# Kernel tuning notes

Measured on AMD Instinct MI355X. Metric: run time of the kernel, lower is better.

Reference implementation:

```python
import jax, jax.numpy as jnp
import numpy as np

M, B, S = 8, 64, 1024
I = K = V = 256
H = 8
F = 1024


def setup_inputs() -> dict:
    key0 = jax.random.key(0)
    ks = iter(jax.random.split(key0, 64))
    nrm = lambda shp, s=1.0: jax.random.normal(next(ks), shp, dtype=jnp.float32) * s
    w = 0.05
    inp = {
        's0': nrm((M, B, I)), 'q0': nrm((M, B, K)), 'k0': nrm((M, B, K)), 'v0': nrm((M, B, V)),
        'key': nrm((S, B, K)), 'value': nrm((S, B, V)),
        'attn_wq': nrm((M, K, K), w), 'attn_wk': nrm((M, K, K), w), 'attn_wv': nrm((M, K, K), w),
        'attn_bq': nrm((M, K), w), 'attn_bk': nrm((M, K), w), 'attn_bv': nrm((M, K), w),
        'attn_wo': nrm((M, K, K), w), 'attn_bo': nrm((M, K), w),
    }
    for p, out in (('q', K), ('k', K), ('v', V), ('s', I)):
        inp[p + '_w1'] = nrm((M, 2 * I, F), w)
        inp[p + '_b1'] = nrm((M, F), w)
        inp[p + '_w2'] = nrm((M, F, out), w)
        inp[p + '_b2'] = nrm((M, out), w)
    inp['g_w1'] = nrm((4, M, 2 * I, F), w)
    inp['g_b1'] = nrm((4, M, F), w)
    inp['g_w2'] = nrm((4, M, F, 1), w)
    inp['g_b2'] = nrm((4, M, 1), w)
    return inp


def _forward(s0, q0, k0, v0, key, value,
             attn_wq, attn_wk, attn_wv, attn_bq, attn_bk, attn_bv, attn_wo, attn_bo,
             q_w1, q_b1, q_w2, q_b2, k_w1, k_b1, k_w2, k_b2,
             v_w1, v_b1, v_w2, v_b2, s_w1, s_b1, s_w2, s_b2,
             g_w1, g_b1, g_w2, g_b2):
    m, b, kd = q0.shape
    s = key.shape[0]
    hd = kd // H
    # per-module projections (single-query decode-style attention)
    q = jnp.einsum('mbk,mkd->mbd', q0, attn_wq) + attn_bq[:, None, :]          # (M,B,K)
    kk = jnp.einsum('sbk,mkd->msbd', key, attn_wk) + attn_bk[:, None, None, :]  # (M,S,B,K)
    vv = jnp.einsum('sbk,mkd->msbd', value, attn_wv) + attn_bv[:, None, None, :]
    qh = q.reshape(m, b, H, hd)
    kh = kk.reshape(m, s, b, H, hd)
    vh = vv.reshape(m, s, b, H, hd)
    scores = jnp.einsum('mbhd,msbhd->mbhs', qh, kh) / jnp.sqrt(jnp.float32(hd))
    aw = jax.nn.softmax(scores, axis=-1)                                        # (M,B,H,S)
    ctx = jnp.einsum('mbhs,msbhd->mbhd', aw, vh).reshape(m, b, kd)
    attn_out = jnp.einsum('mbk,mko->mbo', ctx, attn_wo) + attn_bo[:, None, :]   # (M,B,K)
    attn_weights = aw.mean(axis=2)                                              # (M,B,S)

    # _make_mlp puts ReLU FIRST: Seq(ReLU, Lin, ReLU, Lin, last_act)
    fc_in = jax.nn.relu(jnp.concatenate([attn_out, s0], axis=-1))               # (M,B,2I)

    def head(w1, b1, w2, b2):
        h = jax.nn.relu(jnp.einsum('mbi,mif->mbf', fc_in, w1) + b1[:, None, :])
        return jnp.einsum('mbf,mfo->mbo', h, w2) + b2[:, None, :]

    # non-gate heads: last activation ReLU, then .tanh() in forward
    oq = jnp.tanh(jax.nn.relu(head(q_w1, q_b1, q_w2, q_b2)))
    ok = jnp.tanh(jax.nn.relu(head(k_w1, k_b1, k_w2, k_b2)))
    ov = jnp.tanh(jax.nn.relu(head(v_w1, v_b1, v_w2, v_b2)))
    os_ = jnp.tanh(jax.nn.relu(head(s_w1, s_b1, s_w2, s_b2)))

    # gate heads stacked on leading g axis (query,key,value,state)
    gh = jax.nn.relu(jnp.einsum('mbi,gmif->gmbf', fc_in, g_w1) + g_b1[:, :, None, :])
    gates = jax.nn.sigmoid(jnp.einsum('gmbf,gmfo->gmbo', gh, g_w2) + g_b2[:, :, None, :])
    qg, kg, vg, sg = gates[0], gates[1], gates[2], gates[3]

    gq = qg * oq + (1.0 - qg) * q0
    gk = kg * ok + (1.0 - kg) * k0
    gv = vg * ov + (1.0 - vg) * v0
    gs = sg * os_ + (1.0 - sg) * s0
    return attn_out, attn_weights, gs, gq, gk, gv


def reference(s0, q0, k0, v0, key, value,
              attn_wq, attn_wk, attn_wv, attn_bq, attn_bk, attn_bv, attn_wo, attn_bo,
              q_w1, q_b1, q_w2, q_b2, k_w1, k_b1, k_w2, k_b2,
              v_w1, v_b1, v_w2, v_b2, s_w1, s_b1, s_w2, s_b2,
              g_w1, g_b1, g_w2, g_b2):
    return _forward(s0, q0, k0, v0, key, value,
                    attn_wq, attn_wk, attn_wv, attn_bq, attn_bk, attn_bv, attn_wo, attn_bo,
                    q_w1, q_b1, q_w2, q_b2, k_w1, k_b1, k_w2, k_b2,
                    v_w1, v_b1, v_w2, v_b2, s_w1, s_b1, s_w2, s_b2,
                    g_w1, g_b1, g_w2, g_b2)
```

## Files before the change

kernel.cpp:

```cpp
#include <hip/hip_runtime.h>
#include <math.h>

#define Mm 8
#define Bb 64
#define Ss 1024
#define Kk 256
#define Hh 8
#define HD 32
#define Ff 1024

typedef _Float16 f16x8 __attribute__((ext_vector_type(8)));
typedef float f32x4 __attribute__((ext_vector_type(4)));

#define WS_Q      0u
#define WS_U      131072u
#define WS_QDB    1179648u
#define WS_SC     1183744u
#define WS_WPART  5378048u
#define WS_FC     0u
#define WS_H1     5378048u
#define WS_GATES  262144u
#define WS_HPART  1183744u

__device__ __forceinline__ void dma16(const float* g, float* l) {
  __builtin_amdgcn_global_load_lds(
      (const __attribute__((address_space(1))) unsigned int*)g,
      (__attribute__((address_space(3))) unsigned int*)l, 16, 0, 0);
}

__device__ __forceinline__ f16x8 frag_ctg(const float* T, int r, int quad) {
  const int x = r & 7;
  const float4 a0 = *(const float4*)&T[r * 32 + (((2 * quad) ^ x) << 2)];
  const float4 a1 = *(const float4*)&T[r * 32 + (((2 * quad + 1) ^ x) << 2)];
  f16x8 f;
  f[0] = (_Float16)a0.x; f[1] = (_Float16)a0.y;
  f[2] = (_Float16)a0.z; f[3] = (_Float16)a0.w;
  f[4] = (_Float16)a1.x; f[5] = (_Float16)a1.y;
  f[6] = (_Float16)a1.z; f[7] = (_Float16)a1.w;
  return f;
}

__device__ __forceinline__ int swz(int kr) {
  return (kr & 15) ^ ((kr >> 3) << 1);
}
__device__ __forceinline__ f16x8 frag_ctr(const float* T, int col, int quad) {
  const int g = col >> 2, c = col & 3;
  f16x8 f;
#pragma unroll
  for (int j = 0; j < 8; ++j) {
    const int kr = quad * 8 + j;
    f[j] = (_Float16)T[kr * 64 + ((g ^ swz(kr)) << 2) + c];
  }
  return f;
}

__global__ __launch_bounds__(256) void k1_qproj(
    const float* __restrict__ q0, const float* __restrict__ wq,
    const float* __restrict__ bq, float* __restrict__ qout) {
  __shared__ float q0s[8 * 260];
  const int m = blockIdx.x, b0 = blockIdx.y * 8, t = threadIdx.x;
#pragma unroll
  for (int j = 0; j < 8; ++j)
    q0s[j * 260 + t] = q0[(m * Bb + b0 + j) * Kk + t];
  __syncthreads();
  float acc[8];
  const float bias = bq[m * Kk + t];
#pragma unroll
  for (int j = 0; j < 8; ++j) acc[j] = bias;
  const float* wcol = wq + m * Kk * Kk + t;
  for (int k4 = 0; k4 < Kk / 4; ++k4) {
    const float w0 = wcol[(k4 * 4 + 0) * Kk];
    const float w1 = wcol[(k4 * 4 + 1) * Kk];
    const float w2 = wcol[(k4 * 4 + 2) * Kk];
    const float w3 = wcol[(k4 * 4 + 3) * Kk];
#pragma unroll
    for (int j = 0; j < 8; ++j) {
      const float4 qv = *(const float4*)&q0s[j * 260 + k4 * 4];
      acc[j] += qv.x * w0 + qv.y * w1 + qv.z * w2 + qv.w * w3;
    }
  }
#pragma unroll
  for (int j = 0; j < 8; ++j)
    qout[(m * Bb + b0 + j) * Kk + t] = acc[j];
}

__global__ __launch_bounds__(256) void k2_uproj(
    const float* __restrict__ wk, const float* __restrict__ bk,
    const float* __restrict__ q, float* __restrict__ u,
    float* __restrict__ qdb) {
  __shared__ float qs[64 * 36];
  const int m = blockIdx.x, h = blockIdx.y, t = threadIdx.x;
#pragma unroll
  for (int p = 0; p < 8; ++p) {
    const int idx = p * 256 + t;
    const int d = idx & 31, b = idx >> 5;
    qs[b * 36 + d] = q[(m * Bb + b) * Kk + h * HD + d];
  }
  __syncthreads();
  float acc[64];
#pragma unroll
  for (int b = 0; b < 64; ++b) acc[b] = 0.f;
  const float* wrow = wk + (m * Kk + t) * Kk + h * HD;
#pragma unroll
  for (int d4 = 0; d4 < 8; ++d4) {
    const float4 w4 = *(const float4*)&wrow[d4 * 4];
#pragma unroll
    for (int b = 0; b < 64; ++b) {
      const float4 q4 = *(const float4*)&qs[b * 36 + d4 * 4];
      acc[b] += q4.x * w4.x + q4.y * w4.y + q4.z * w4.z + q4.w * w4.w;
    }
  }
  for (int b = 0; b < 64; ++b)
    u[((m * Bb + b) * Hh + h) * Kk + t] = acc[b];
  if (t < 64) {
    float s = 0.f;
#pragma unroll
    for (int d = 0; d < 32; ++d)
      s += qs[t * 36 + d] * bk[m * Kk + h * HD + d];
    qdb[(m * Bb + t) * Hh + h] = s;
  }
}

__global__ __launch_bounds__(256) void k3_scores(
    const float* __restrict__ key, const float* __restrict__ u,
    const float* __restrict__ qdb, float* __restrict__ sc) {
  __shared__ __attribute__((aligned(16))) float TA[2][2048];
  __shared__ __attribute__((aligned(16))) float TB[2][2048];
  __shared__ float qd[64];
  const int b = blockIdx.x, st0 = blockIdx.y * 64, t = threadIdx.x;
  const int w = t >> 6, lane = t & 63, quad = (t >> 4) & 3, l15 = t & 15;
  if (t < 64) qd[t] = qdb[((t >> 3) * Bb + b) * Hh + (t & 7)];

  auto dmaAB = [&](int c, int buf) {
#pragma unroll
    for (int j = 0; j < 2; ++j) {
      const int r = w * 16 + j * 8 + (lane >> 3);
      const int gp = (lane & 7) ^ (r & 7);
      dma16(u + (((r >> 3) * Bb + b) * Hh + (r & 7)) * Kk + c * 32 + gp * 4,
            &TA[buf][(w * 2 + j) * 256 + lane * 4]);
    }
#pragma unroll
    for (int j = 0; j < 2; ++j) {
      const int sr = w * 16 + j * 8 + (lane >> 3);
      const int gp = (lane & 7) ^ (sr & 7);
      dma16(key + (size_t)(st0 + sr) * (Bb * Kk) + b * Kk + c * 32 + gp * 4,
            &TB[buf][(w * 2 + j) * 256 + lane * 4]);
    }
  };

  f32x4 acc[4];
#pragma unroll
  for (int i = 0; i < 4; ++i) acc[i] = (f32x4){0.f, 0.f, 0.f, 0.f};
  dmaAB(0, 0);
  __syncthreads();
#pragma unroll
  for (int c = 0; c < 8; ++c) {
    if (c + 1 < 8) dmaAB(c + 1, (c + 1) & 1);
    const float* A = TA[c & 1];
    const float* B = TB[c & 1];
    const f16x8 af = frag_ctg(A, w * 16 + l15, quad);
#pragma unroll
    for (int sf = 0; sf < 4; ++sf) {
      const f16x8 bf = frag_ctg(B, sf * 16 + l15, quad);
      acc[sf] =
          __builtin_amdgcn_mfma_f32_16x16x32_f16(af, bf, acc[sf], 0, 0, 0);
    }
    __syncthreads();
  }
  const float scale = 0.17677669529663687f;
#pragma unroll
  for (int sf = 0; sf < 4; ++sf) {
    const int s = st0 + sf * 16 + l15;
#pragma unroll
    for (int r = 0; r < 4; ++r) {
      const int mh = w * 16 + quad * 4 + r;
      sc[(size_t)(((mh >> 3) * Bb + b) * Hh + (mh & 7)) * Ss + s] =
          (acc[sf][r] + qd[mh]) * scale;
    }
  }
}

__global__ __launch_bounds__(256) void k3b_softmax(float* __restrict__ sc,
                                                   float* __restrict__ out) {
  __shared__ float rows[8 * 1024];
  const int m = blockIdx.x, b = blockIdx.y, t = threadIdx.x;
  const int w = t >> 6, lane = t & 63;
  const size_t base = (size_t)(m * Bb + b) * (Hh * Ss);
#pragma unroll
  for (int hh = 0; hh < 2; ++hh) {
    const int h = w * 2 + hh;
    float* g = sc + base + h * 1024;
    float4 v0 = *(const float4*)&g[lane * 4];
    float4 v1 = *(const float4*)&g[256 + lane * 4];
    float4 v2 = *(const float4*)&g[512 + lane * 4];
    float4 v3 = *(const float4*)&g[768 + lane * 4];
    float mx = fmaxf(fmaxf(fmaxf(v0.x, v0.y), fmaxf(v0.z, v0.w)),
                     fmaxf(fmaxf(v1.x, v1.y), fmaxf(v1.z, v1.w)));
    mx = fmaxf(mx, fmaxf(fmaxf(fmaxf(v2.x, v2.y), fmaxf(v2.z, v2.w)),
                         fmaxf(fmaxf(v3.x, v3.y), fmaxf(v3.z, v3.w))));
#pragma unroll
    for (int off = 32; off > 0; off >>= 1)
      mx = fmaxf(mx, __shfl_xor(mx, off, 64));
    v0.x = __expf(v0.x - mx); v0.y = __expf(v0.y - mx);
    v0.z = __expf(v0.z - mx); v0.w = __expf(v0.w - mx);
    v1.x = __expf(v1.x - mx); v1.y = __expf(v1.y - mx);
    v1.z = __expf(v1.z - mx); v1.w = __expf(v1.w - mx);
    v2.x = __expf(v2.x - mx); v2.y = __expf(v2.y - mx);
    v2.z = __expf(v2.z - mx); v2.w = __expf(v2.w - mx);
    v3.x = __expf(v3.x - mx); v3.y = __expf(v3.y - mx);
    v3.z = __expf(v3.z - mx); v3.w = __expf(v3.w - mx);
    float sm = v0.x + v0.y + v0.z + v0.w + v1.x + v1.y + v1.z + v1.w +
               v2.x + v2.y + v2.z + v2.w + v3.x + v3.y + v3.z + v3.w;
#pragma unroll
    for (int off = 32; off > 0; off >>= 1) sm += __shfl_xor(sm, off, 64);
    const float inv = 1.f / sm;
    v0.x *= inv; v0.y *= inv; v0.z *= inv; v0.w *= inv;
    v1.x *= inv; v1.y *= inv; v1.z *= inv; v1.w *= inv;
    v2.x *= inv; v2.y *= inv; v2.z *= inv; v2.w *= inv;
    v3.x *= inv; v3.y *= inv; v3.z *= inv; v3.w *= inv;
    *(float4*)&g[lane * 4] = v0;
    *(float4*)&g[256 + lane * 4] = v1;
    *(float4*)&g[512 + lane * 4] = v2;
    *(float4*)&g[768 + lane * 4] = v3;
    float* r = rows + h * 1024;
    *(float4*)&r[lane * 4] = v0;
    *(float4*)&r[256 + lane * 4] = v1;
    *(float4*)&r[512 + lane * 4] = v2;
    *(float4*)&r[768 + lane * 4] = v3;
  }
  __syncthreads();
#pragma unroll
  for (int p = 0; p < 4; ++p) {
    const int s = p * 256 + t;
    float sum = 0.f;
#pragma unroll
    for (int h = 0; h < 8; ++h) sum += rows[h * 1024 + s];
    out[131072u + (m * Bb + b) * Ss + s] = sum * 0.125f;
  }
}

__global__ __launch_bounds__(256) void k4a_av(const float* __restrict__ value,
                                              const float* __restrict__ aw,
                                              float* __restrict__ wpart) {
  __shared__ __attribute__((aligned(16))) float TA[2][2048];
  __shared__ __attribute__((aligned(16))) float TB[2][2048];
  const int b = blockIdx.x, ko = blockIdx.y, sq = blockIdx.z, t = threadIdx.x;
  const int w = t >> 6, lane = t & 63, quad = (t >> 4) & 3, l15 = t & 15;

  auto dmaAB = [&](int c, int buf) {
#pragma unroll
    for (int j = 0; j < 2; ++j) {
      const int r = w * 16 + j * 8 + (lane >> 3);
      const int gp = (lane & 7) ^ (r & 7);
      dma16(aw + ((size_t)((r >> 3) * Bb + b) * Hh + (r & 7)) * Ss +
                sq * 256 + c * 32 + gp * 4,
            &TA[buf][(w * 2 + j) * 256 + lane * 4]);
    }
#pragma unroll
    for (int j = 0; j < 2; ++j) {
      const int kr = w * 8 + j * 4 + (lane >> 4);
      const int gp = (lane & 15) ^ swz(kr);
      dma16(value + (size_t)(sq * 256 + c * 32 + kr) * (Bb * Kk) + b * Kk +
                ko * 64 + gp * 4,
            &TB[buf][(w * 2 + j) * 256 + lane * 4]);
    }
  };

  f32x4 acc[4];
#pragma unroll
  for (int i = 0; i < 4; ++i) acc[i] = (f32x4){0.f, 0.f, 0.f, 0.f};
  dmaAB(0, 0);
  __syncthreads();
#pragma unroll
  for (int c = 0; c < 8; ++c) {
    if (c + 1 < 8) dmaAB(c + 1, (c + 1) & 1);
    const float* A = TA[c & 1];
    const float* B = TB[c & 1];
    const f16x8 af = frag_ctg(A, w * 16 + l15, quad);
#pragma unroll
    for (int nf = 0; nf < 4; ++nf) {
      const f16x8 bf = frag_ctr(B, nf * 16 + l15, quad);
      acc[nf] =
          __builtin_amdgcn_mfma_f32_16x16x32_f16(af, bf, acc[nf], 0, 0, 0);
    }
    __syncthreads();
  }
  float* wp = wpart + sq * 1048576u;
#pragma unroll
  for (int nf = 0; nf < 4; ++nf) {
    const int k = ko * 64 + nf * 16 + l15;
#pragma unroll
    for (int r = 0; r < 4; ++r) {
      const int mh = w * 16 + quad * 4 + r;
      wp[((size_t)((mh >> 3) * Bb + b) * Hh + (mh & 7)) * Kk + k] =
          acc[nf][r];
    }
  }
}

__global__ __launch_bounds__(256) void k5_ctx(
    const float* __restrict__ wv, const float* __restrict__ bv,
    const float* __restrict__ wo, const float* __restrict__ bo,
    const float* __restrict__ s0in, const float* __restrict__ wpart,
    float* __restrict__ attn_out, float* __restrict__ fc) {
  __shared__ float wsh[2048];
  __shared__ float ctxs[256];
  const int m = blockIdx.x, b = blockIdx.y, t = threadIdx.x;
  const int base = (m * Bb + b) * (Hh * Kk);
#pragma unroll
  for (int p = 0; p < 8; ++p) {
    const int o = base + p * 256 + t;
    wsh[p * 256 + t] = wpart[o] + wpart[1048576u + o] + wpart[2097152u + o] +
                       wpart[3145728u + o];
  }
  __syncthreads();
  const int h = t >> 5;
  float acc = bv[m * Kk + t];
  const float* wvc = wv + m * Kk * Kk + t;
  for (int k4 = 0; k4 < 64; ++k4) {
    const float4 a4 = *(const float4*)&wsh[h * 256 + k4 * 4];
    acc += a4.x * wvc[(k4 * 4 + 0) * Kk] + a4.y * wvc[(k4 * 4 + 1) * Kk] +
           a4.z * wvc[(k4 * 4 + 2) * Kk] + a4.w * wvc[(k4 * 4 + 3) * Kk];
  }
  ctxs[t] = acc;
  __syncthreads();
  float acc2 = bo[m * Kk + t];
  const float* woc = wo + m * Kk * Kk + t;
  for (int k4 = 0; k4 < 64; ++k4) {
    const float4 c4 = *(const float4*)&ctxs[k4 * 4];
    acc2 += c4.x * woc[(k4 * 4 + 0) * Kk] + c4.y * woc[(k4 * 4 + 1) * Kk] +
            c4.z * woc[(k4 * 4 + 2) * Kk] + c4.w * woc[(k4 * 4 + 3) * Kk];
  }
  const int ob = (m * Bb + b) * Kk + t;
  attn_out[ob] = acc2;
  fc[(m * Bb + b) * 512 + t] = fmaxf(acc2, 0.f);
  fc[(m * Bb + b) * 512 + 256 + t] = fmaxf(s0in[ob], 0.f);
}

__global__ __launch_bounds__(256) void k6_mlp1(
    const float* __restrict__ fc, const float* __restrict__ w1q,
    const float* __restrict__ w1k, const float* __restrict__ w1v,
    const float* __restrict__ w1s, const float* __restrict__ w1g,
    const float* __restrict__ b1q, const float* __restrict__ b1k,
    const float* __restrict__ b1v, const float* __restrict__ b1s,
    const float* __restrict__ b1g, float* __restrict__ h1) {
  __shared__ __attribute__((aligned(16))) float TA[2][2048];
  __shared__ __attribute__((aligned(16))) float TB[2][2048];
  const int ft = blockIdx.x, m = blockIdx.y, head = blockIdx.z,
            t = threadIdx.x;
  const float* w1;
  const float* b1;
  if (head == 0)      { w1 = w1q; b1 = b1q; }
  else if (head == 1) { w1 = w1k; b1 = b1k; }
  else if (head == 2) { w1 = w1v; b1 = b1v; }
  else if (head == 3) { w1 = w1s; b1 = b1s; }
  else {
    w1 = w1g + (size_t)(head - 4) * (Mm * 512 * Ff);
    b1 = b1g + (head - 4) * (Mm * Ff);
  }
  w1 += (size_t)m * 512 * Ff;
  b1 += m * Ff;
  const int w = t >> 6, lane = t & 63, quad = (t >> 4) & 3, l15 = t & 15;
  const float* fcm = fc + m * Bb * 512;

  auto dmaAB = [&](int c, int buf) {
#pragma unroll
    for (int j = 0; j < 2; ++j) {
      const int r = w * 16 + j * 8 + (lane >> 3);
      const int gp = (lane & 7) ^ (r & 7);
      dma16(fcm + r * 512 + c * 32 + gp * 4,
            &TA[buf][(w * 2 + j) * 256 + lane * 4]);
    }
#pragma unroll
    for (int j = 0; j < 2; ++j) {
      const int kr = w * 8 + j * 4 + (lane >> 4);
      const int gp = (lane & 15) ^ swz(kr);
      dma16(w1 + (size_t)(c * 32 + kr) * Ff + ft * 64 + gp * 4,
            &TB[buf][(w * 2 + j) * 256 + lane * 4]);
    }
  };

  f32x4 acc[4];
#pragma unroll
  for (int i = 0; i < 4; ++i) acc[i] = (f32x4){0.f, 0.f, 0.f, 0.f};
  dmaAB(0, 0);
  __syncthreads();
#pragma unroll
  for (int c = 0; c < 16; ++c) {
    if (c + 1 < 16) dmaAB(c + 1, (c + 1) & 1);
    const float* A = TA[c & 1];
    const float* B = TB[c & 1];
    const f16x8 bf = frag_ctr(B, w * 16 + l15, quad);
#pragma unroll
    for (int mt = 0; mt < 4; ++mt) {
      const f16x8 af = frag_ctg(A, mt * 16 + l15, quad);
      acc[mt] =
          __builtin_amdgcn_mfma_f32_16x16x32_f16(af, bf, acc[mt], 0, 0, 0);
    }
    __syncthreads();
  }
  const int f = ft * 64 + w * 16 + l15;
  const float bias = b1[f];
  float* hb = h1 + (size_t)((head * Mm + m) * Bb) * Ff + f;
#pragma unroll
  for (int mt = 0; mt < 4; ++mt) {
#pragma unroll
    for (int r = 0; r < 4; ++r) {
      const int bb = mt * 16 + quad * 4 + r;
      hb[(size_t)bb * Ff] = fmaxf(acc[mt][r] + bias, 0.f);
    }
  }
}

__global__ __launch_bounds__(64) void k6b_gates(
    const float* __restrict__ h1, const float* __restrict__ gw2,
    const float* __restrict__ gb2, float* __restrict__ gates) {
  const int gm = blockIdx.x, b = blockIdx.y, t = threadIdx.x;
  const int g = gm >> 3, m = gm & 7;
  const float* hrow = h1 + (size_t)(((4 + g) * Mm + m) * Bb + b) * Ff;
  const float* wrow = gw2 + (g * Mm + m) * Ff;
  float s = 0.f;
#pragma unroll
  for (int i = 0; i < 16; ++i) s += hrow[t + i * 64] * wrow[t + i * 64];
  for (int off = 32; off > 0; off >>= 1) s += __shfl_down(s, off, 64);
  if (t == 0)
    gates[(g * Mm + m) * Bb + b] =
        1.f / (1.f + __expf(-(s + gb2[g * Mm + m])));
}

__global__ __launch_bounds__(256) void k7a_mlp2(
    const float* __restrict__ h1, const float* __restrict__ w2q,
    const float* __restrict__ w2k, const float* __restrict__ w2v,
    const float* __restrict__ w2s, float* __restrict__ hpart) {
  __shared__ __attribute__((aligned(16))) float TA[2][2048];
  __shared__ __attribute__((aligned(16))) float TB[2][2048];
  const int ot = blockIdx.x & 3, fq = blockIdx.x >> 2;
  const int m = blockIdx.y, head = blockIdx.z, t = threadIdx.x;
  const float* w2 =
      (head == 0) ? w2q : (head == 1) ? w2k : (head == 2) ? w2v : w2s;
  w2 += (size_t)m * Ff * Kk;
  const int w = t >> 6, lane = t & 63, quad = (t >> 4) & 3, l15 = t & 15;
  const float* hbase = h1 + (size_t)((head * Mm + m) * Bb) * Ff + fq * 256;

  auto dmaAB = [&](int c, int buf) {
#pragma unroll
    for (int j = 0; j < 2; ++j) {
      const int r = w * 16 + j * 8 + (lane >> 3);
      const int gp = (lane & 7) ^ (r & 7);
      dma16(hbase + (size_t)r * Ff + c * 32 + gp * 4,
            &TA[buf][(w * 2 + j) * 256 + lane * 4]);
    }
#pragma unroll
    for (int j = 0; j < 2; ++j) {
      const int kr = w * 8 + j * 4 + (lane >> 4);
      const int gp = (lane & 15) ^ swz(kr);
      dma16(w2 + (size_t)(fq * 256 + c * 32 + kr) * Kk + ot * 64 + gp * 4,
            &TB[buf][(w * 2 + j) * 256 + lane * 4]);
    }
  };

  f32x4 acc[4];
#pragma unroll
  for (int i = 0; i < 4; ++i) acc[i] = (f32x4){0.f, 0.f, 0.f, 0.f};
  dmaAB(0, 0);
  __syncthreads();
#pragma unroll
  for (int c = 0; c < 8; ++c) {
    if (c + 1 < 8) dmaAB(c + 1, (c + 1) & 1);
    const float* A = TA[c & 1];
    const float* B = TB[c & 1];
    const f16x8 bf = frag_ctr(B, w * 16 + l15, quad);
#pragma unroll
    for (int mt = 0; mt < 4; ++mt) {
      const f16x8 af = frag_ctg(A, mt * 16 + l15, quad);
      acc[mt] =
          __builtin_amdgcn_mfma_f32_16x16x32_f16(af, bf, acc[mt], 0, 0, 0);
    }
    __syncthreads();
  }
  const int o = ot * 64 + w * 16 + l15;
  float* hp = hpart + fq * 524288u + (size_t)((head * Mm + m) * Bb) * Kk + o;
#pragma unroll
  for (int mt = 0; mt < 4; ++mt) {
#pragma unroll
    for (int r = 0; r < 4; ++r) {
      const int bb = mt * 16 + quad * 4 + r;
      hp[(size_t)bb * Kk] = acc[mt][r];
    }
  }
}

__global__ __launch_bounds__(256) void k7b_final(
    const float* __restrict__ hpart, const float* __restrict__ gates,
    const float* __restrict__ b2q, const float* __restrict__ b2k,
    const float* __restrict__ b2v, const float* __restrict__ b2s,
    const float* __restrict__ q0, const float* __restrict__ k0,
    const float* __restrict__ v0, const float* __restrict__ s0,
    float* __restrict__ out) {
  const int idx = blockIdx.x * 256 + threadIdx.x;
  const int o = idx & 255;
  const int b = (idx >> 8) & 63;
  const int m = (idx >> 14) & 7;
  const int head = idx >> 17;
  const float* b2 = (head == 0) ? b2q : (head == 1) ? b2k
                    : (head == 2) ? b2v : b2s;
  const float* x0 = (head == 0) ? q0 : (head == 1) ? k0
                    : (head == 2) ? v0 : s0;
  const unsigned ooff = (head == 0) ? 786432u
                        : (head == 1) ? 917504u
                        : (head == 2) ? 1048576u : 655360u;
  float v = hpart[idx] + hpart[524288u + idx] + hpart[1048576u + idx] +
            hpart[1572864u + idx] + b2[m * Kk + o];
  v = tanhf(fmaxf(v, 0.f));
  const float g = gates[(head * Mm + m) * Bb + b];
  const float x = x0[(m * Bb + b) * Kk + o];
  out[ooff + (m * Bb + b) * Kk + o] = g * v + (1.f - g) * x;
}

extern "C" void kernel_launch(void* const* d_in, const int* in_sizes, int n_in,
                              void* d_out, int out_size, void* d_ws,
                              size_t ws_size, hipStream_t stream) {
  (void)in_sizes; (void)n_in; (void)out_size; (void)ws_size;
  const float* s0  = (const float*)d_in[0];
  const float* q0  = (const float*)d_in[1];
  const float* k0  = (const float*)d_in[2];
  const float* v0  = (const float*)d_in[3];
  const float* key = (const float*)d_in[4];
  const float* val = (const float*)d_in[5];
  const float* wq  = (const float*)d_in[6];
  const float* wk  = (const float*)d_in[7];
  const float* wv  = (const float*)d_in[8];
  const float* bqa = (const float*)d_in[9];
  const float* bka = (const float*)d_in[10];
  const float* bva = (const float*)d_in[11];
  const float* wo  = (const float*)d_in[12];
  const float* bo  = (const float*)d_in[13];
  const float* qw1 = (const float*)d_in[14];
  const float* qb1 = (const float*)d_in[15];
  const float* qw2 = (const float*)d_in[16];
  const float* qb2 = (const float*)d_in[17];
  const float* kw1 = (const float*)d_in[18];
  const float* kb1 = (const float*)d_in[19];
  const float* kw2 = (const float*)d_in[20];
  const float* kb2 = (const float*)d_in[21];
  const float* vw1 = (const float*)d_in[22];
  const float* vb1 = (const float*)d_in[23];
  const float* vw2 = (const float*)d_in[24];
  const float* vb2 = (const float*)d_in[25];
  const float* sw1 = (const float*)d_in[26];
  const float* sb1 = (const float*)d_in[27];
  const float* sw2 = (const float*)d_in[28];
  const float* sb2 = (const float*)d_in[29];
  const float* gw1 = (const float*)d_in[30];
  const float* gb1 = (const float*)d_in[31];
  const float* gw2 = (const float*)d_in[32];
  const float* gb2 = (const float*)d_in[33];
  float* ws  = (float*)d_ws;
  float* out = (float*)d_out;

  k1_qproj<<<dim3(8, 8), 256, 0, stream>>>(q0, wq, bqa, ws + WS_Q);
  k2_uproj<<<dim3(8, 8), 256, 0, stream>>>(wk, bka, ws + WS_Q, ws + WS_U,
                                           ws + WS_QDB);
  k3_scores<<<dim3(64, 16), 256, 0, stream>>>(key, ws + WS_U, ws + WS_QDB,
                                              ws + WS_SC);
  k3b_softmax<<<dim3(8, 64), 256, 0, stream>>>(ws + WS_SC, out);
  k4a_av<<<dim3(64, 4, 4), 256, 0, stream>>>(val, ws + WS_SC, ws + WS_WPART);
  k5_ctx<<<dim3(8, 64), 256, 0, stream>>>(wv, bva, wo, bo, s0, ws + WS_WPART,
                                          out, ws + WS_FC);
  k6_mlp1<<<dim3(16, 8, 8), 256, 0, stream>>>(ws + WS_FC, qw1, kw1, vw1, sw1,
                                              gw1, qb1, kb1, vb1, sb1, gb1,
                                              ws + WS_H1);
  k6b_gates<<<dim3(32, 64), 64, 0, stream>>>(ws + WS_H1, gw2, gb2,
                                             ws + WS_GATES);
  k7a_mlp2<<<dim3(16, 8, 4), 256, 0, stream>>>(ws + WS_H1, qw2, kw2, vw2, sw2,
                                               ws + WS_HPART);
  k7b_final<<<dim3(2048), 256, 0, stream>>>(ws + WS_HPART, ws + WS_GATES, qb2,
                                            kb2, vb2, sb2, q0, k0, v0, s0,
                                            out);
}
```

Measured before the change: 431.3 us.

## Store intermediates in fp16 and load MFMA fragments directly from global memory

Scores, attention weights, the fc input and the hidden MLP activations are now stored in half precision in the workspace instead of fp32, which halves their memory traffic. All MFMA kernels drop their double-buffered LDS staging via global_load_lds and load fragments straight from global memory into registers, removing LDS use and barriers. The cost is uncoalesced strided global loads for column-oriented operands (value, w1, w2), with each element read separately. Per-warp data reuse that LDS used to provide is also lost, and fp16 intermediates reduce precision.

```diff
diff --git a/kernel.cpp b/kernel.cpp
--- a/kernel.cpp
+++ b/kernel.cpp
@@ -13,46 +13,14 @@
 typedef float f32x4 __attribute__((ext_vector_type(4)));
 
 #define WS_Q      0u
+#define WS_FC16   0u
 #define WS_U      131072u
+#define WS_GATES  131072u
 #define WS_QDB    1179648u
-#define WS_SC     1183744u
-#define WS_WPART  5378048u
-#define WS_FC     0u
-#define WS_H1     5378048u
-#define WS_GATES  262144u
+#define WS_SC16   1183744u
 #define WS_HPART  1183744u
-
-__device__ __forceinline__ void dma16(const float* g, float* l) {
-  __builtin_amdgcn_global_load_lds(
-      (const __attribute__((address_space(1))) unsigned int*)g,
-      (__attribute__((address_space(3))) unsigned int*)l, 16, 0, 0);
-}
-
-__device__ __forceinline__ f16x8 frag_ctg(const float* T, int r, int quad) {
-  const int x = r & 7;
-  const float4 a0 = *(const float4*)&T[r * 32 + (((2 * quad) ^ x) << 2)];
-  const float4 a1 = *(const float4*)&T[r * 32 + (((2 * quad + 1) ^ x) << 2)];
-  f16x8 f;
-  f[0] = (_Float16)a0.x; f[1] = (_Float16)a0.y;
-  f[2] = (_Float16)a0.z; f[3] = (_Float16)a0.w;
-  f[4] = (_Float16)a1.x; f[5] = (_Float16)a1.y;
-  f[6] = (_Float16)a1.z; f[7] = (_Float16)a1.w;
-  return f;
-}
-
-__device__ __forceinline__ int swz(int kr) {
-  return (kr & 15) ^ ((kr >> 3) << 1);
-}
-__device__ __forceinline__ f16x8 frag_ctr(const float* T, int col, int quad) {
-  const int g = col >> 2, c = col & 3;
-  f16x8 f;
-#pragma unroll
-  for (int j = 0; j < 8; ++j) {
-    const int kr = quad * 8 + j;
-    f[j] = (_Float16)T[kr * 64 + ((g ^ swz(kr)) << 2) + c];
-  }
-  return f;
-}
+#define WS_WPART  3280896u
+#define WS_H116   3280896u
 
 __global__ __launch_bounds__(256) void k1_qproj(
     const float* __restrict__ q0, const float* __restrict__ wq,
@@ -123,64 +91,53 @@
 
 __global__ __launch_bounds__(256) void k3_scores(
     const float* __restrict__ key, const float* __restrict__ u,
-    const float* __restrict__ qdb, float* __restrict__ sc) {
-  __shared__ __attribute__((aligned(16))) float TA[2][2048];
-  __shared__ __attribute__((aligned(16))) float TB[2][2048];
-  __shared__ float qd[64];
+    const float* __restrict__ qdb, _Float16* __restrict__ scH) {
   const int b = blockIdx.x, st0 = blockIdx.y * 64, t = threadIdx.x;
-  const int w = t >> 6, lane = t & 63, quad = (t >> 4) & 3, l15 = t & 15;
-  if (t < 64) qd[t] = qdb[((t >> 3) * Bb + b) * Hh + (t & 7)];
-
-  auto dmaAB = [&](int c, int buf) {
-#pragma unroll
-    for (int j = 0; j < 2; ++j) {
-      const int r = w * 16 + j * 8 + (lane >> 3);
-      const int gp = (lane & 7) ^ (r & 7);
-      dma16(u + (((r >> 3) * Bb + b) * Hh + (r & 7)) * Kk + c * 32 + gp * 4,
-            &TA[buf][(w * 2 + j) * 256 + lane * 4]);
-    }
-#pragma unroll
-    for (int j = 0; j < 2; ++j) {
-      const int sr = w * 16 + j * 8 + (lane >> 3);
-      const int gp = (lane & 7) ^ (sr & 7);
-      dma16(key + (size_t)(st0 + sr) * (Bb * Kk) + b * Kk + c * 32 + gp * 4,
-            &TB[buf][(w * 2 + j) * 256 + lane * 4]);
-    }
-  };
-
+  const int w = t >> 6, quad = (t >> 4) & 3, l15 = t & 15;
+  const int mh = w * 16 + l15;
+  const float* up = u + (((mh >> 3) * Bb + b) * Hh + (mh & 7)) * Kk;
   f32x4 acc[4];
 #pragma unroll
   for (int i = 0; i < 4; ++i) acc[i] = (f32x4){0.f, 0.f, 0.f, 0.f};
-  dmaAB(0, 0);
-  __syncthreads();
 #pragma unroll
   for (int c = 0; c < 8; ++c) {
-    if (c + 1 < 8) dmaAB(c + 1, (c + 1) & 1);
-    const float* A = TA[c & 1];
-    const float* B = TB[c & 1];
-    const f16x8 af = frag_ctg(A, w * 16 + l15, quad);
+    const float* ua = up + c * 32 + quad * 8;
+    const float4 a0 = *(const float4*)ua;
+    const float4 a1 = *(const float4*)(ua + 4);
+    f16x8 af;
+    af[0] = (_Float16)a0.x; af[1] = (_Float16)a0.y;
+    af[2] = (_Float16)a0.z; af[3] = (_Float16)a0.w;
+    af[4] = (_Float16)a1.x; af[5] = (_Float16)a1.y;
+    af[6] = (_Float16)a1.z; af[7] = (_Float16)a1.w;
 #pragma unroll
     for (int sf = 0; sf < 4; ++sf) {
-      const f16x8 bf = frag_ctg(B, sf * 16 + l15, quad);
+      const float* kp = key + (size_t)(st0 + sf * 16 + l15) * (Bb * Kk) +
+                        b * Kk + c * 32 + quad * 8;
+      const float4 b0 = *(const float4*)kp;
+      const float4 b1 = *(const float4*)(kp + 4);
+      f16x8 bf;
+      bf[0] = (_Float16)b0.x; bf[1] = (_Float16)b0.y;
+      bf[2] = (_Float16)b0.z; bf[3] = (_Float16)b0.w;
+      bf[4] = (_Float16)b1.x; bf[5] = (_Float16)b1.y;
+      bf[6] = (_Float16)b1.z; bf[7] = (_Float16)b1.w;
       acc[sf] =
           __builtin_amdgcn_mfma_f32_16x16x32_f16(af, bf, acc[sf], 0, 0, 0);
     }
-    __syncthreads();
   }
   const float scale = 0.17677669529663687f;
 #pragma unroll
-  for (int sf = 0; sf < 4; ++sf) {
-    const int s = st0 + sf * 16 + l15;
-#pragma unroll
-    for (int r = 0; r < 4; ++r) {
-      const int mh = w * 16 + quad * 4 + r;
-      sc[(size_t)(((mh >> 3) * Bb + b) * Hh + (mh & 7)) * Ss + s] =
-          (acc[sf][r] + qd[mh]) * scale;
-    }
-  }
-}
-
-__global__ __launch_bounds__(256) void k3b_softmax(float* __restrict__ sc,
+  for (int r = 0; r < 4; ++r) {
+    const int mo = w * 16 + quad * 4 + r;
+    const size_t row = (size_t)(((mo >> 3) * Bb + b) * Hh + (mo & 7));
+    const float qd = qdb[row];
+#pragma unroll
+    for (int sf = 0; sf < 4; ++sf)
+      scH[row * Ss + st0 + sf * 16 + l15] =
+          (_Float16)((acc[sf][r] + qd) * scale);
+  }
+}
+
+__global__ __launch_bounds__(256) void k3b_softmax(_Float16* __restrict__ scH,
                                                    float* __restrict__ out) {
   __shared__ float rows[8 * 1024];
   const int m = blockIdx.x, b = blockIdx.y, t = threadIdx.x;
@@ -189,44 +146,40 @@
 #pragma unroll
   for (int hh = 0; hh < 2; ++hh) {
     const int h = w * 2 + hh;
-    float* g = sc + base + h * 1024;
-    float4 v0 = *(const float4*)&g[lane * 4];
-    float4 v1 = *(const float4*)&g[256 + lane * 4];
-    float4 v2 = *(const float4*)&g[512 + lane * 4];
-    float4 v3 = *(const float4*)&g[768 + lane * 4];
-    float mx = fmaxf(fmaxf(fmaxf(v0.x, v0.y), fmaxf(v0.z, v0.w)),
-                     fmaxf(fmaxf(v1.x, v1.y), fmaxf(v1.z, v1.w)));
-    mx = fmaxf(mx, fmaxf(fmaxf(fmaxf(v2.x, v2.y), fmaxf(v2.z, v2.w)),
-                         fmaxf(fmaxf(v3.x, v3.y), fmaxf(v3.z, v3.w))));
+    _Float16* g = scH + base + h * 1024;
+    const f16x8 x0 = *(const f16x8*)&g[lane * 8];
+    const f16x8 x1 = *(const f16x8*)&g[512 + lane * 8];
+    float v[16];
+#pragma unroll
+    for (int i = 0; i < 8; ++i) { v[i] = (float)x0[i]; v[8 + i] = (float)x1[i]; }
+    float mx = v[0];
+#pragma unroll
+    for (int i = 1; i < 16; ++i) mx = fmaxf(mx, v[i]);
 #pragma unroll
     for (int off = 32; off > 0; off >>= 1)
       mx = fmaxf(mx, __shfl_xor(mx, off, 64));
-    v0.x = __expf(v0.x - mx); v0.y = __expf(v0.y - mx);
-    v0.z = __expf(v0.z - mx); v0.w = __expf(v0.w - mx);
-    v1.x = __expf(v1.x - mx); v1.y = __expf(v1.y - mx);
-    v1.z = __expf(v1.z - mx); v1.w = __expf(v1.w - mx);
-    v2.x = __expf(v2.x - mx); v2.y = __expf(v2.y - mx);
-    v2.z = __expf(v2.z - mx); v2.w = __expf(v2.w - mx);
-    v3.x = __expf(v3.x - mx); v3.y = __expf(v3.y - mx);
-    v3.z = __expf(v3.z - mx); v3.w = __expf(v3.w - mx);
-    float sm = v0.x + v0.y + v0.z + v0.w + v1.x + v1.y + v1.z + v1.w +
-               v2.x + v2.y + v2.z + v2.w + v3.x + v3.y + v3.z + v3.w;
+    float sm = 0.f;
+#pragma unroll
+    for (int i = 0; i < 16; ++i) { v[i] = __expf(v[i] - mx); sm += v[i]; }
 #pragma unroll
     for (int off = 32; off > 0; off >>= 1) sm += __shfl_xor(sm, off, 64);
     const float inv = 1.f / sm;
-    v0.x *= inv; v0.y *= inv; v0.z *= inv; v0.w *= inv;
-    v1.x *= inv; v1.y *= inv; v1.z *= inv; v1.w *= inv;
-    v2.x *= inv; v2.y *= inv; v2.z *= inv; v2.w *= inv;
-    v3.x *= inv; v3.y *= inv; v3.z *= inv; v3.w *= inv;
-    *(float4*)&g[lane * 4] = v0;
-    *(float4*)&g[256 + lane * 4] = v1;
-    *(float4*)&g[512 + lane * 4] = v2;
-    *(float4*)&g[768 + lane * 4] = v3;
+    f16x8 y0, y1;
+#pragma unroll
+    for (int i = 0; i < 16; ++i) v[i] *= inv;
+#pragma unroll
+    for (int i = 0; i < 8; ++i) {
+      y0[i] = (_Float16)v[i];
+      y1[i] = (_Float16)v[8 + i];
+    }
+    *(f16x8*)&g[lane * 8] = y0;
+    *(f16x8*)&g[512 + lane * 8] = y1;
     float* r = rows + h * 1024;
-    *(float4*)&r[lane * 4] = v0;
-    *(float4*)&r[256 + lane * 4] = v1;
-    *(float4*)&r[512 + lane * 4] = v2;
-    *(float4*)&r[768 + lane * 4] = v3;
+#pragma unroll
+    for (int i = 0; i < 8; ++i) {
+      r[lane * 8 + i] = v[i];
+      r[512 + lane * 8 + i] = v[8 + i];
+    }
   }
   __syncthreads();
 #pragma unroll
@@ -240,50 +193,31 @@
 }
 
 __global__ __launch_bounds__(256) void k4a_av(const float* __restrict__ value,
-                                              const float* __restrict__ aw,
+                                              const _Float16* __restrict__ awH,
                                               float* __restrict__ wpart) {
-  __shared__ __attribute__((aligned(16))) float TA[2][2048];
-  __shared__ __attribute__((aligned(16))) float TB[2][2048];
   const int b = blockIdx.x, ko = blockIdx.y, sq = blockIdx.z, t = threadIdx.x;
-  const int w = t >> 6, lane = t & 63, quad = (t >> 4) & 3, l15 = t & 15;
-
-  auto dmaAB = [&](int c, int buf) {
-#pragma unroll
-    for (int j = 0; j < 2; ++j) {
-      const int r = w * 16 + j * 8 + (lane >> 3);
-      const int gp = (lane & 7) ^ (r & 7);
-      dma16(aw + ((size_t)((r >> 3) * Bb + b) * Hh + (r & 7)) * Ss +
-                sq * 256 + c * 32 + gp * 4,
-            &TA[buf][(w * 2 + j) * 256 + lane * 4]);
-    }
-#pragma unroll
-    for (int j = 0; j < 2; ++j) {
-      const int kr = w * 8 + j * 4 + (lane >> 4);
-      const int gp = (lane & 15) ^ swz(kr);
-      dma16(value + (size_t)(sq * 256 + c * 32 + kr) * (Bb * Kk) + b * Kk +
-                ko * 64 + gp * 4,
-            &TB[buf][(w * 2 + j) * 256 + lane * 4]);
-    }
-  };
-
+  const int w = t >> 6, quad = (t >> 4) & 3, l15 = t & 15;
+  const int mh = w * 16 + l15;
+  const _Float16* ap =
+      awH + ((size_t)((mh >> 3) * Bb + b) * Hh + (mh & 7)) * Ss + sq * 256;
   f32x4 acc[4];
 #pragma unroll
   for (int i = 0; i < 4; ++i) acc[i] = (f32x4){0.f, 0.f, 0.f, 0.f};
-  dmaAB(0, 0);
-  __syncthreads();
 #pragma unroll
   for (int c = 0; c < 8; ++c) {
-    if (c + 1 < 8) dmaAB(c + 1, (c + 1) & 1);
-    const float* A = TA[c & 1];
-    const float* B = TB[c & 1];
-    const f16x8 af = frag_ctg(A, w * 16 + l15, quad);
+    const f16x8 af = *(const f16x8*)&ap[c * 32 + quad * 8];
 #pragma unroll
     for (int nf = 0; nf < 4; ++nf) {
-      const f16x8 bf = frag_ctr(B, nf * 16 + l15, quad);
+      const int k = ko * 64 + nf * 16 + l15;
+      f16x8 bf;
+#pragma unroll
+      for (int j = 0; j < 8; ++j)
+        bf[j] = (_Float16)value[(size_t)(sq * 256 + c * 32 + quad * 8 + j) *
+                                    (Bb * Kk) +
+                                b * Kk + k];
       acc[nf] =
           __builtin_amdgcn_mfma_f32_16x16x32_f16(af, bf, acc[nf], 0, 0, 0);
     }
-    __syncthreads();
   }
   float* wp = wpart + sq * 1048576u;
 #pragma unroll
@@ -291,8 +225,8 @@
     const int k = ko * 64 + nf * 16 + l15;
 #pragma unroll
     for (int r = 0; r < 4; ++r) {
-      const int mh = w * 16 + quad * 4 + r;
-      wp[((size_t)((mh >> 3) * Bb + b) * Hh + (mh & 7)) * Kk + k] =
+      const int mo = w * 16 + quad * 4 + r;
+      wp[((size_t)((mo >> 3) * Bb + b) * Hh + (mo & 7)) * Kk + k] =
           acc[nf][r];
     }
   }
@@ -302,7 +236,7 @@
     const float* __restrict__ wv, const float* __restrict__ bv,
     const float* __restrict__ wo, const float* __restrict__ bo,
     const float* __restrict__ s0in, const float* __restrict__ wpart,
-    float* __restrict__ attn_out, float* __restrict__ fc) {
+    float* __restrict__ attn_out, _Float16* __restrict__ fcH) {
   __shared__ float wsh[2048];
   __shared__ float ctxs[256];
   const int m = blockIdx.x, b = blockIdx.y, t = threadIdx.x;
@@ -333,19 +267,17 @@
   }
   const int ob = (m * Bb + b) * Kk + t;
   attn_out[ob] = acc2;
-  fc[(m * Bb + b) * 512 + t] = fmaxf(acc2, 0.f);
-  fc[(m * Bb + b) * 512 + 256 + t] = fmaxf(s0in[ob], 0.f);
+  fcH[(m * Bb + b) * 512 + t] = (_Float16)fmaxf(acc2, 0.f);
+  fcH[(m * Bb + b) * 512 + 256 + t] = (_Float16)fmaxf(s0in[ob], 0.f);
 }
 
 __global__ __launch_bounds__(256) void k6_mlp1(
-    const float* __restrict__ fc, const float* __restrict__ w1q,
+    const _Float16* __restrict__ fcH, const float* __restrict__ w1q,
     const float* __restrict__ w1k, const float* __restrict__ w1v,
     const float* __restrict__ w1s, const float* __restrict__ w1g,
     const float* __restrict__ b1q, const float* __restrict__ b1k,
     const float* __restrict__ b1v, const float* __restrict__ b1s,
-    const float* __restrict__ b1g, float* __restrict__ h1) {
-  __shared__ __attribute__((aligned(16))) float TA[2][2048];
-  __shared__ __attribute__((aligned(16))) float TB[2][2048];
+    const float* __restrict__ b1g, _Float16* __restrict__ h1H) {
   const int ft = blockIdx.x, m = blockIdx.y, head = blockIdx.z,
             t = threadIdx.x;
   const float* w1;
@@ -360,68 +292,53 @@
   }
   w1 += (size_t)m * 512 * Ff;
   b1 += m * Ff;
-  const int w = t >> 6, lane = t & 63, quad = (t >> 4) & 3, l15 = t & 15;
-  const float* fcm = fc + m * Bb * 512;
-
-  auto dmaAB = [&](int c, int buf) {
-#pragma unroll
-    for (int j = 0; j < 2; ++j) {
-      const int r = w * 16 + j * 8 + (lane >> 3);
-      const int gp = (lane & 7) ^ (r & 7);
-      dma16(fcm + r * 512 + c * 32 + gp * 4,
-            &TA[buf][(w * 2 + j) * 256 + lane * 4]);
-    }
-#pragma unroll
-    for (int j = 0; j < 2; ++j) {
-      const int kr = w * 8 + j * 4 + (lane >> 4);
-      const int gp = (lane & 15) ^ swz(kr);
-      dma16(w1 + (size_t)(c * 32 + kr) * Ff + ft * 64 + gp * 4,
-            &TB[buf][(w * 2 + j) * 256 + lane * 4]);
-    }
-  };
-
+  const int w = t >> 6, quad = (t >> 4) & 3, l15 = t & 15;
+  const int f = ft * 64 + w * 16 + l15;
+  const float* wp = w1 + f;
+  const _Float16* ap = fcH + (size_t)m * Bb * 512;
   f32x4 acc[4];
 #pragma unroll
   for (int i = 0; i < 4; ++i) acc[i] = (f32x4){0.f, 0.f, 0.f, 0.f};
-  dmaAB(0, 0);
-  __syncthreads();
 #pragma unroll
   for (int c = 0; c < 16; ++c) {
-    if (c + 1 < 16) dmaAB(c + 1, (c + 1) & 1);
-    const float* A = TA[c & 1];
-    const float* B = TB[c & 1];
-    const f16x8 bf = frag_ctr(B, w * 16 + l15, quad);
-#pragma unroll
-    for (int mt = 0; mt < 4; ++mt) {
-      const f16x8 af = frag_ctg(A, mt * 16 + l15, quad);
+    float bw[8];
+#pragma unroll
+    for (int j = 0; j < 8; ++j)
+      bw[j] = wp[(size_t)(c * 32 + quad * 8 + j) * Ff];
+    f16x8 af[4];
+#pragma unroll
+    for (int mt = 0; mt < 4; ++mt)
+      af[mt] =
+          *(const f16x8*)&ap[(mt * 16 + l15) * 512 + c * 32 + quad * 8];
+    f16x8 bf;
+#pragma unroll
+    for (int j = 0; j < 8; ++j) bf[j] = (_Float16)bw[j];
+#pragma unroll
+    for (int mt = 0; mt < 4; ++mt)
       acc[mt] =
-          __builtin_amdgcn_mfma_f32_16x16x32_f16(af, bf, acc[mt], 0, 0, 0);
-    }
-    __syncthreads();
-  }
-  const int f = ft * 64 + w * 16 + l15;
+          __builtin_amdgcn_mfma_f32_16x16x32_f16(af[mt], bf, acc[mt], 0, 0, 0);
+  }
   const float bias = b1[f];
-  float* hb = h1 + (size_t)((head * Mm + m) * Bb) * Ff + f;
-#pragma unroll
-  for (int mt = 0; mt < 4; ++mt) {
-#pragma unroll
-    for (int r = 0; r < 4; ++r) {
-      const int bb = mt * 16 + quad * 4 + r;
-      hb[(size_t)bb * Ff] = fmaxf(acc[mt][r] + bias, 0.f);
-    }
-  }
+  _Float16* hb = h1H + (size_t)((head * Mm + m) * Bb) * Ff + f;
+#pragma unroll
+  for (int mt = 0; mt < 4; ++mt)
+#pragma unroll
+    for (int r = 0; r < 4; ++r)
+      hb[(size_t)(mt * 16 + quad * 4 + r) * Ff] =
+          (_Float16)fmaxf(acc[mt][r] + bias, 0.f);
 }
 
 __global__ __launch_bounds__(64) void k6b_gates(
-    const float* __restrict__ h1, const float* __restrict__ gw2,
+    const _Float16* __restrict__ h1H, const float* __restrict__ gw2,
     const float* __restrict__ gb2, float* __restrict__ gates) {
   const int gm = blockIdx.x, b = blockIdx.y, t = threadIdx.x;
   const int g = gm >> 3, m = gm & 7;
-  const float* hrow = h1 + (size_t)(((4 + g) * Mm + m) * Bb + b) * Ff;
+  const _Float16* hrow = h1H + (size_t)(((4 + g) * Mm + m) * Bb + b) * Ff;
   const float* wrow = gw2 + (g * Mm + m) * Ff;
   float s = 0.f;
 #pragma unroll
-  for (int i = 0; i < 16; ++i) s += hrow[t + i * 64] * wrow[t + i * 64];
+  for (int i = 0; i < 16; ++i)
+    s += (float)hrow[t + i * 64] * wrow[t + i * 64];
   for (int off = 32; off > 0; off >>= 1) s += __shfl_down(s, off, 64);
   if (t == 0)
     gates[(g * Mm + m) * Bb + b] =
@@ -429,65 +346,46 @@
 }
 
 __global__ __launch_bounds__(256) void k7a_mlp2(
-    const float* __restrict__ h1, const float* __restrict__ w2q,
+    const _Float16* __restrict__ h1H, const float* __restrict__ w2q,
     const float* __restrict__ w2k, const float* __restrict__ w2v,
     const float* __restrict__ w2s, float* __restrict__ hpart) {
-  __shared__ __attribute__((aligned(16))) float TA[2][2048];
-  __shared__ __attribute__((aligned(16))) float TB[2][2048];
   const int ot = blockIdx.x & 3, fq = blockIdx.x >> 2;
   const int m = blockIdx.y, head = blockIdx.z, t = threadIdx.x;
   const float* w2 =
       (head == 0) ? w2q : (head == 1) ? w2k : (head == 2) ? w2v : w2s;
   w2 += (size_t)m * Ff * Kk;
-  const int w = t >> 6, lane = t & 63, quad = (t >> 4) & 3, l15 = t & 15;
-  const float* hbase = h1 + (size_t)((head * Mm + m) * Bb) * Ff + fq * 256;
-
-  auto dmaAB = [&](int c, int buf) {
-#pragma unroll
-    for (int j = 0; j < 2; ++j) {
-      const int r = w * 16 + j * 8 + (lane >> 3);
-      const int gp = (lane & 7) ^ (r & 7);
-      dma16(hbase + (size_t)r * Ff + c * 32 + gp * 4,
-            &TA[buf][(w * 2 + j) * 256 + lane * 4]);
-    }
-#pragma unroll
-    for (int j = 0; j < 2; ++j) {
-      const int kr = w * 8 + j * 4 + (lane >> 4);
-      const int gp = (lane & 15) ^ swz(kr);
-      dma16(w2 + (size_t)(fq * 256 + c * 32 + kr) * Kk + ot * 64 + gp * 4,
-            &TB[buf][(w * 2 + j) * 256 + lane * 4]);
-    }
-  };
-
+  const int w = t >> 6, quad = (t >> 4) & 3, l15 = t & 15;
+  const int o = ot * 64 + w * 16 + l15;
+  const float* wp = w2 + (size_t)(fq * 256) * Kk + o;
+  const _Float16* ap = h1H + (size_t)((head * Mm + m) * Bb) * Ff + fq * 256;
   f32x4 acc[4];
 #pragma unroll
   for (int i = 0; i < 4; ++i) acc[i] = (f32x4){0.f, 0.f, 0.f, 0.f};
-  dmaAB(0, 0);
-  __syncthreads();
 #pragma unroll
   for (int c = 0; c < 8; ++c) {
-    if (c + 1 < 8) dmaAB(c + 1, (c + 1) & 1);
-    const float* A = TA[c & 1];
-    const float* B = TB[c & 1];
-    const f16x8 bf = frag_ctr(B, w * 16 + l15, quad);
-#pragma unroll
-    for (int mt = 0; mt < 4; ++mt) {
-      const f16x8 af = frag_ctg(A, mt * 16 + l15, quad);
+    float bw[8];
+#pragma unroll
+    for (int j = 0; j < 8; ++j)
+      bw[j] = wp[(size_t)(c * 32 + quad * 8 + j) * Kk];
+    f16x8 af[4];
+#pragma unroll
+    for (int mt = 0; mt < 4; ++mt)
+      af[mt] =
+          *(const f16x8*)&ap[(size_t)(mt * 16 + l15) * Ff + c * 32 + quad * 8];
+    f16x8 bf;
+#pragma unroll
+    for (int j = 0; j < 8; ++j) bf[j] = (_Float16)bw[j];
+#pragma unroll
+    for (int mt = 0; mt < 4; ++mt)
       acc[mt] =
-          __builtin_amdgcn_mfma_f32_16x16x32_f16(af, bf, acc[mt], 0, 0, 0);
-    }
-    __syncthreads();
-  }
-  const int o = ot * 64 + w * 16 + l15;
+          __builtin_amdgcn_mfma_f32_16x16x32_f16(af[mt], bf, acc[mt], 0, 0, 0);
+  }
   float* hp = hpart + fq * 524288u + (size_t)((head * Mm + m) * Bb) * Kk + o;
 #pragma unroll
-  for (int mt = 0; mt < 4; ++mt) {
-#pragma unroll
-    for (int r = 0; r < 4; ++r) {
-      const int bb = mt * 16 + quad * 4 + r;
-      hp[(size_t)bb * Kk] = acc[mt][r];
-    }
-  }
+  for (int mt = 0; mt < 4; ++mt)
+#pragma unroll
+    for (int r = 0; r < 4; ++r)
+      hp[(size_t)(mt * 16 + quad * 4 + r) * Kk] = acc[mt][r];
 }
 
 __global__ __launch_bounds__(256) void k7b_final(
@@ -557,22 +455,23 @@
   const float* gb2 = (const float*)d_in[33];
   float* ws  = (float*)d_ws;
   float* out = (float*)d_out;
+  _Float16* scH = (_Float16*)(ws + WS_SC16);
+  _Float16* fcH = (_Float16*)(ws + WS_FC16);
+  _Float16* h1H = (_Float16*)(ws + WS_H116);
 
   k1_qproj<<<dim3(8, 8), 256, 0, stream>>>(q0, wq, bqa, ws + WS_Q);
   k2_uproj<<<dim3(8, 8), 256, 0, stream>>>(wk, bka, ws + WS_Q, ws + WS_U,
                                            ws + WS_QDB);
   k3_scores<<<dim3(64, 16), 256, 0, stream>>>(key, ws + WS_U, ws + WS_QDB,
-                                              ws + WS_SC);
-  k3b_softmax<<<dim3(8, 64), 256, 0, stream>>>(ws + WS_SC, out);
-  k4a_av<<<dim3(64, 4, 4), 256, 0, stream>>>(val, ws + WS_SC, ws + WS_WPART);
+                                              scH);
+  k3b_softmax<<<dim3(8, 64), 256, 0, stream>>>(scH, out);
+  k4a_av<<<dim3(64, 4, 4), 256, 0, stream>>>(val, scH, ws + WS_WPART);
   k5_ctx<<<dim3(8, 64), 256, 0, stream>>>(wv, bva, wo, bo, s0, ws + WS_WPART,
-                                          out, ws + WS_FC);
-  k6_mlp1<<<dim3(16, 8, 8), 256, 0, stream>>>(ws + WS_FC, qw1, kw1, vw1, sw1,
-                                              gw1, qb1, kb1, vb1, sb1, gb1,
-                                              ws + WS_H1);
-  k6b_gates<<<dim3(32, 64), 64, 0, stream>>>(ws + WS_H1, gw2, gb2,
-                                             ws + WS_GATES);
-  k7a_mlp2<<<dim3(16, 8, 4), 256, 0, stream>>>(ws + WS_H1, qw2, kw2, vw2, sw2,
+                                          out, fcH);
+  k6_mlp1<<<dim3(16, 8, 8), 256, 0, stream>>>(fcH, qw1, kw1, vw1, sw1, gw1,
+                                              qb1, kb1, vb1, sb1, gb1, h1H);
+  k6b_gates<<<dim3(32, 64), 64, 0, stream>>>(h1H, gw2, gb2, ws + WS_GATES);
+  k7a_mlp2<<<dim3(16, 8, 4), 256, 0, stream>>>(h1H, qw2, kw2, vw2, sw2,
                                                ws + WS_HPART);
   k7b_final<<<dim3(2048), 256, 0, stream>>>(ws + WS_HPART, ws + WS_GATES, qb2,
                                             kb2, vb2, sb2, q0, k0, v0, s0,
```

After: 458.2 us. +6.2%, slower.
